# Kernel optimization log

Hardware: AMD Instinct MI355X
Metric: run time of the kernel (lower is better)

The kernel has to match this reference:

```python
import jax, jax.numpy as jnp
import numpy as np
import math

B, N, H, NH, L, NC = 8, 128, 128, 4, 4, 1
DH = H // NH
EPS = 1e-5

def _gelu(x):
    return jax.nn.gelu(x, approximate=False)  # torch nn.GELU default is exact erf

def _ln(x, g, b):
    m = x.mean(-1, keepdims=True)
    v = ((x - m) ** 2).mean(-1, keepdims=True)
    return (x - m) / jnp.sqrt(v + EPS) * g + b

def _bn(x, mask, g, b):
    # BatchNorm1d over valid (unpadded) nodes only, batch statistics (train mode)
    m = mask[..., None].astype(x.dtype)
    cnt = m.sum()
    mu = (x * m).sum((0, 1)) / cnt
    var = (((x - mu) ** 2) * m).sum((0, 1)) / cnt
    return (x - mu) / jnp.sqrt(var + EPS) * g + b

def _forward(e, u, atom_emb, bond_emb, eigw_W, eigw_b, mha_norm_g, mha_norm_b, qkv_W, qkv_b, out_W, out_b, ffn_norm_g, ffn_norm_b, ffn1_W, ffn1_b, ffn2_W, ffn2_b, dec_W, dec_b, fe1_W, fe1_b, fe2_W, fe2_b, pre_W, pre_b, f1_W, f1_b, bn1_g, bn1_b, f2_W, f2_b, bn2_g, bn2_b, lin_W, lin_b, node_feat, edge_feat, length):
    Bx, Nx = e.shape
    node_mask = jnp.arange(Nx)[None, :] < length[:, None]                        # [B,N]
    edge_mask = (node_mask[:, :, None] & node_mask[:, None, :]).astype(e.dtype)  # [B,src,dst]
    # SineEncoding
    div = jnp.exp(jnp.arange(0, H, 2, dtype=e.dtype) * (-math.log(10000.0) / H))
    pe = (e * 100.0)[:, :, None] * div
    eeig = jnp.concatenate([e[..., None], jnp.sin(pe), jnp.cos(pe)], axis=-1)    # [B,N,H+1]
    eig = eeig @ eigw_W.T + eigw_b                                               # [B,N,H]
    # multi-head self-attention over eigenvalue tokens with key padding mask
    xm = _ln(eig, mha_norm_g, mha_norm_b)
    qkv = xm @ qkv_W.T + qkv_b
    q, k, v = jnp.split(qkv, 3, axis=-1)
    q = q.reshape(Bx, Nx, NH, DH).transpose(0, 2, 1, 3)
    k = k.reshape(Bx, Nx, NH, DH).transpose(0, 2, 1, 3)
    v = v.reshape(Bx, Nx, NH, DH).transpose(0, 2, 1, 3)
    scores = jnp.einsum('bhqd,bhkd->bhqk', q, k) / math.sqrt(DH)
    scores = jnp.where(node_mask[:, None, None, :], scores, -jnp.inf)
    attn = jax.nn.softmax(scores, axis=-1)                                       # [B,NH,N,N]
    ctx = jnp.einsum('bhqk,bhkd->bhqd', attn, v).transpose(0, 2, 1, 3).reshape(Bx, Nx, H)
    eig = eig + (ctx @ out_W.T + out_b)
    y = _ln(eig, ffn_norm_g, ffn_norm_b)
    y = _gelu(y @ ffn1_W.T + ffn1_b) @ ffn2_W.T + ffn2_b
    eig = eig + y
    new_e = (eig @ dec_W.T + dec_b).transpose(0, 2, 1)                           # [B,NH,N]
    # spectral bases: identity + u @ diag(new_e_k) @ u^T per head, as fused diagonal scale
    filters = jnp.einsum('bnm,bkm,bpm->bnpk', u, new_e, u)                       # [B,N,N,NH]
    eye = jnp.broadcast_to(jnp.eye(Nx, dtype=e.dtype)[None, :, :, None], (Bx, Nx, Nx, 1))
    bases = jnp.concatenate([eye, filters], axis=-1)                             # [B,N,N,NH+1]
    bases = _gelu(_gelu(bases @ fe1_W.T + fe1_b) @ fe2_W.T + fe2_b)              # [B,N,N,H]
    xf = atom_emb[node_feat]                                                     # [B,N,H]
    ea = bond_emb[edge_feat]                                                     # [B,N,N,H]
    for l in range(L):
        # copy_u gather + per-edge FFN * bases + masked scatter-sum to dst
        msg = _gelu((xf[:, :, None, :] + ea) @ pre_W[l].T + pre_b[l]) * bases
        aggr = jnp.einsum('bijh,bij->bjh', msg, edge_mask)
        xf = xf + aggr
        y = xf @ f1_W[l].T + f1_b[l]
        y = jax.nn.relu(_bn(y, node_mask, bn1_g[l], bn1_b[l]))
        y = y @ f2_W[l].T + f2_b[l]
        y = jax.nn.relu(_bn(y, node_mask, bn2_g[l], bn2_b[l]))
        xf = xf + y
    nm = node_mask[..., None].astype(e.dtype)
    h = (xf * nm).sum(1) / length[:, None].astype(e.dtype)                       # AvgPooling over valid nodes
    h = h @ lin_W.T + lin_b
    return h, new_e, attn

def setup_inputs():
    key = jax.random.key(0)
    ks = iter(jax.random.split(key, 64))
    def w(*shape):
        return jax.random.normal(next(ks), shape, dtype=jnp.float32) * 0.02
    z = lambda *s: jnp.zeros(s, dtype=jnp.float32)
    o = lambda *s: jnp.ones(s, dtype=jnp.float32)
    e = jax.random.uniform(next(ks), (B, N), dtype=jnp.float32) * 2.0
    u = jnp.linalg.qr(jax.random.normal(next(ks), (B, N, N), dtype=jnp.float32))[0]
    inp = {
        'e': e, 'u': u,
        'atom_emb': w(40, H), 'bond_emb': w(10, H).at[0].set(0.0),
        'eigw_W': w(H, H + 1), 'eigw_b': z(H),
        'mha_norm_g': o(H), 'mha_norm_b': z(H),
        'qkv_W': w(3 * H, H), 'qkv_b': z(3 * H),
        'out_W': w(H, H), 'out_b': z(H),
        'ffn_norm_g': o(H), 'ffn_norm_b': z(H),
        'ffn1_W': w(H, H), 'ffn1_b': z(H),
        'ffn2_W': w(H, H), 'ffn2_b': z(H),
        'dec_W': w(NH, H), 'dec_b': z(NH),
        'fe1_W': w(H, NH + 1), 'fe1_b': z(H),
        'fe2_W': w(H, H), 'fe2_b': z(H),
        'pre_W': w(L, H, H), 'pre_b': z(L, H),
        'f1_W': w(L, H, H), 'f1_b': z(L, H),
        'bn1_g': o(L, H), 'bn1_b': z(L, H),
        'f2_W': w(L, H, H), 'f2_b': z(L, H),
        'bn2_g': o(L, H), 'bn2_b': z(L, H),
        'lin_W': w(NC, H), 'lin_b': z(NC),
        'node_feat': jax.random.randint(next(ks), (B, N), 0, 40),
        'edge_feat': jax.random.randint(next(ks), (B, N, N), 0, 10),
        'length': 64 + jax.random.randint(next(ks), (B,), 0, N - 63),
    }
    return inp

def reference(e, u, atom_emb, bond_emb, eigw_W, eigw_b, mha_norm_g, mha_norm_b, qkv_W, qkv_b, out_W, out_b, ffn_norm_g, ffn_norm_b, ffn1_W, ffn1_b, ffn2_W, ffn2_b, dec_W, dec_b, fe1_W, fe1_b, fe2_W, fe2_b, pre_W, pre_b, f1_W, f1_b, bn1_g, bn1_b, f2_W, f2_b, bn2_g, bn2_b, lin_W, lin_b, node_feat, edge_feat, length):
    return _forward(e, u, atom_emb, bond_emb, eigw_W, eigw_b, mha_norm_g, mha_norm_b, qkv_W, qkv_b, out_W, out_b, ffn_norm_g, ffn_norm_b, ffn1_W, ffn1_b, ffn2_W, ffn2_b, dec_W, dec_b, fe1_W, fe1_b, fe2_W, fe2_b, pre_W, pre_b, f1_W, f1_b, bn1_g, bn1_b, f2_W, f2_b, bn2_g, bn2_b, lin_W, lin_b, node_feat, edge_feat, length)
```

## Files before the change

### kernel.cpp

```cpp
#include <hip/hip_runtime.h>
#include <hip/hip_bf16.h>
#include <math.h>

#define BB 8
#define NN 128
#define HH 128
#define NHD 4
#define DHD 32
#define LAY 4
#define EPSV 1e-5f

typedef __hip_bfloat16 bf16;
typedef unsigned short ushortt;
typedef short bf16x8 __attribute__((ext_vector_type(8)));
typedef float f32x4 __attribute__((ext_vector_type(4)));

__device__ __forceinline__ float b2f(bf16 x){ return __bfloat162float(x); }
__device__ __forceinline__ bf16 f2b(float x){ return __float2bfloat16(x); }
__device__ __forceinline__ ushortt f2us(float x){ bf16 b=__float2bfloat16(x); return *(ushortt*)&b; }
__device__ __forceinline__ float gelu_f(float x){ return 0.5f*x*(1.0f+erff(x*0.7071067811865476f)); }
__device__ __forceinline__ float gelu_h(float x){
  float t = 0.7978845608028654f*x*(1.0f + 0.044715f*x*x);
  float e = __expf(2.0f*t);
  float th = 1.0f - 2.0f/(e + 1.0f);
  return 0.5f*x*(1.0f + th);
}
__device__ __forceinline__ float erf_fast(float x){
  float ax = fabsf(x);
  float t = __builtin_amdgcn_rcpf(__builtin_fmaf(0.3275911f, ax, 1.0f));
  float p = __builtin_fmaf(1.061405429f, t, -1.453152027f);
  p = __builtin_fmaf(p, t, 1.421413741f);
  p = __builtin_fmaf(p, t, -0.284496736f);
  p = __builtin_fmaf(p, t, 0.254829592f);
  p = p*t;
  float e = __expf(-ax*ax);
  float y = __builtin_fmaf(-p, e, 1.0f);
  return __builtin_copysignf(y, x);
}
__device__ __forceinline__ float gelu_fe(float x){
  return 0.5f*x*(1.0f + erf_fast(x*0.7071067811865476f));
}


__global__ __launch_bounds__(256) void k_prep(const float* __restrict__ fe2W,
    const float* __restrict__ preW, const float* __restrict__ eigW,
    const float* __restrict__ qkvW, const float* __restrict__ outW,
    const float* __restrict__ ffn1W, const float* __restrict__ ffn2W,
    const float* __restrict__ f1W, const float* __restrict__ f2W,
    const float* __restrict__ aemb, const int* __restrict__ nf,
    const float* __restrict__ bemb, const float* __restrict__ preb,
    ushortt* __restrict__ wbf, float* __restrict__ gs, float* __restrict__ xf0,
    float* __restrict__ eigWT, float* __restrict__ qkvWT, float* __restrict__ outWT,
    float* __restrict__ ffn1WT, float* __restrict__ ffn2WT,
    float* __restrict__ f1WT, float* __restrict__ f2WT,
    float* __restrict__ bondWall){
  int idx = blockIdx.x*256 + threadIdx.x;
  if (idx < 10240) gs[idx] = 0.f;
  if (idx < 81920){
    float v = (idx < 16384) ? fe2W[idx] : preW[idx - 16384];
    wbf[idx] = f2us(v);
  }
  if (idx < 131072){
    int node = idx >> 7, h2 = idx & 127;
    xf0[idx] = aemb[nf[node]*HH + h2];
  }
  if (idx < 16512){ int o = idx/129, kq = idx - o*129; eigWT[kq*128+o] = eigW[idx]; }
  if (idx < 49152){ int o = idx>>7, m = idx&127; qkvWT[m*384+o] = qkvW[idx]; }
  if (idx < 16384){ int o = idx>>7, m = idx&127;
    outWT[m*128+o]  = outW[idx];
    ffn1WT[m*128+o] = ffn1W[idx];
    ffn2WT[m*128+o] = ffn2W[idx];
  }
  if (idx < 65536){ int l = idx>>14, r = idx&16383; int o = r>>7, m = r&127;
    f1WT[l*16384 + m*128+o] = f1W[idx];
    f2WT[l*16384 + m*128+o] = f2W[idx];
  }
  if (idx < 5120){
    int l = idx / 1280; int r = idx - l*1280; int e2 = r >> 7; int hcol = r & 127;
    const float* br = bemb + e2*128;
    const float* wr = preW + l*16384 + hcol*128;
    float acc = preb[l*128 + hcol];
    for (int m=0;m<128;m++) acc += br[m]*wr[m];
    bondWall[idx] = acc;
  }
}


__global__ void k_fe_a(const float* __restrict__ e, const float* __restrict__ eigWT,
                       const float* __restrict__ eigb, const float* __restrict__ g,
                       const float* __restrict__ bt, const float* __restrict__ qkvWT,
                       const float* __restrict__ qkvb,
                       float* __restrict__ eigout, float* __restrict__ q,
                       float* __restrict__ kT, float* __restrict__ v){
  int row = blockIdx.x; int tid = threadIdx.x;
  int b = row >> 7, n = row & 127;
  __shared__ float ee[129]; __shared__ float buf[128]; __shared__ float xm[128];
  float ev = e[row];
  if (tid < 64){
    float dv = expf(-0.1439115683121279f * (float)tid);
    float pe = ev * 100.0f * dv;
    ee[1+tid] = sinf(pe);
    ee[65+tid] = cosf(pe);
  }
  if (tid == 0) ee[0] = ev;
  __syncthreads();
  float x = eigb[tid];
  for (int k2=0;k2<129;k2++) x += ee[k2]*eigWT[k2*128+tid];
  eigout[row*HH+tid] = x;
  buf[tid]=x; __syncthreads();
  for (int s2=64;s2>0;s2>>=1){ if(tid<s2) buf[tid]+=buf[tid+s2]; __syncthreads(); }
  float mean = buf[0]*(1.0f/128.0f); __syncthreads();
  float d = x-mean; buf[tid]=d*d; __syncthreads();
  for (int s2=64;s2>0;s2>>=1){ if(tid<s2) buf[tid]+=buf[tid+s2]; __syncthreads(); }
  float var = buf[0]*(1.0f/128.0f);
  xm[tid] = d*rsqrtf(var+EPSV)*g[tid]+bt[tid];
  __syncthreads();
  #pragma unroll
  for (int s3=0;s3<3;s3++){
    float acc = qkvb[s3*HH+tid];
    const float* wt = qkvWT + s3*HH + tid;
    for (int m=0;m<HH;m++) acc += xm[m]*wt[m*384];
    if (s3==0) q[row*HH+tid]=acc;
    else if (s3==1) kT[b*16384 + tid*128 + n]=acc;
    else v[row*HH+tid]=acc;
  }
}

__global__ __launch_bounds__(512) void k_attc(const float* __restrict__ q,
    const float* __restrict__ kT, const float* __restrict__ v,
    const float* __restrict__ eig, const int* __restrict__ length,
    const float* __restrict__ outWT, const float* __restrict__ outb,
    const float* __restrict__ fng, const float* __restrict__ fnb,
    const float* __restrict__ w1T, const float* __restrict__ b1,
    const float* __restrict__ w2T, const float* __restrict__ b2,
    const float* __restrict__ dW, const float* __restrict__ db,
    float* __restrict__ newe, float* __restrict__ outp){
  int row = blockIdx.x; int b = row>>7, qi = row&127;
  int tid = threadIdx.x;
  int hg = tid>>7, lt = tid&127;
  int len = length[b];
  __shared__ float qv[4][DHD];
  __shared__ float red[4][128];
  __shared__ float satt[4][128];
  __shared__ float sc[128], sbuf[128], sxm[128], stt[128], sx[128];
  if (lt < DHD) qv[hg][lt] = q[(b*NN+qi)*HH + hg*DHD + lt];
  __syncthreads();
  float s = -1e30f;
  if (lt < len){
    const float* kr = kT + b*16384 + hg*DHD*128 + lt;
    float scr=0.f;
    for (int d2=0; d2<DHD; d2++) scr += qv[hg][d2]*kr[d2*128];
    s = scr * 0.17677669529663687f;
  }
  red[hg][lt]=s; __syncthreads();
  for (int st=64;st>0;st>>=1){ if(lt<st) red[hg][lt]=fmaxf(red[hg][lt],red[hg][lt+st]); __syncthreads(); }
  float mx = red[hg][0]; __syncthreads();
  float pp = (lt<len)? expf(s-mx):0.0f;
  red[hg][lt]=pp; __syncthreads();
  for (int st=64;st>0;st>>=1){ if(lt<st) red[hg][lt]+=red[hg][lt+st]; __syncthreads(); }
  float a = pp / red[hg][0];
  satt[hg][lt] = a;
  outp[4104 + ((b*NHD+hg)*NN+qi)*NN + lt] = a;
  __syncthreads();
  if (tid < 128){
    int hd = tid>>5;
    float acc=0.f;
    for (int j=0;j<NN;j++) acc += satt[hd][j]*v[(b*NN+j)*HH+tid];
    sc[tid]=acc;
  }
  __syncthreads();
  if (tid < 128){
    float o = outb[tid];
    for (int m=0;m<HH;m++) o += sc[m]*outWT[m*128+tid];
    float x = eig[row*HH+tid] + o;
    sx[tid] = x; sbuf[tid] = x;
  }
  __syncthreads();
  for (int s2=64;s2>0;s2>>=1){ if(tid<s2) sbuf[tid]+=sbuf[tid+s2]; __syncthreads(); }
  float mean = sbuf[0]*(1.f/128.f); __syncthreads();
  if (tid < 128){ float d = sx[tid]-mean; sbuf[tid]=d*d; }
  __syncthreads();
  for (int s2=64;s2>0;s2>>=1){ if(tid<s2) sbuf[tid]+=sbuf[tid+s2]; __syncthreads(); }
  float var = sbuf[0]*(1.f/128.f);
  if (tid < 128){
    float d = sx[tid]-mean;
    sxm[tid] = d*rsqrtf(var+EPSV)*fng[tid]+fnb[tid];
  }
  __syncthreads();
  if (tid < 128){
    float a1=b1[tid];
    for (int m=0;m<HH;m++) a1+=sxm[m]*w1T[m*128+tid];
    stt[tid]=gelu_f(a1);
  }
  __syncthreads();
  if (tid < 128){
    float a2=b2[tid];
    for (int m=0;m<HH;m++) a2+=stt[m]*w2T[m*128+tid];
    sx[tid] = sx[tid] + a2;
  }
  __syncthreads();
  if (tid < 4){
    float acc = db[tid];
    const float* wr = dW + tid*HH;
    for (int h2=0;h2<HH;h2++) acc += sx[h2]*wr[h2];
    int idx=(b*NHD+tid)*NN+qi;
    newe[idx]=acc; outp[8+idx]=acc;
  }
}

__global__ __launch_bounds__(256) void k_fe2(const float* __restrict__ u,
    const float* __restrict__ newe,
    const float* __restrict__ w1g, const float* __restrict__ b1g,
    const ushortt* __restrict__ w2bf, const float* __restrict__ b2g,
    const int* __restrict__ length,
    bf16* __restrict__ bases){
  int blk = blockIdx.x;
  int bi = blk >> 1;
  int r0 = (blk & 1)*64;
  int b = bi >> 7;
  int nloc = bi & 127;
  int len = length[b];
  if (nloc >= len || r0 >= len) return;
  int tid = threadIdx.x;
  int lane = tid & 63, w = tid >> 6, quad = lane >> 4, l15 = lane & 15;
  int pr = r0 + w*16 + l15;
  __shared__ alignas(16) ushortt sW2[128*128];
  __shared__ float w1a[128*4];
  __shared__ float w1b[128*2];
  __shared__ float b2s[128];
  __shared__ float cn[4][128];
  for (int idx = tid; idx < 2048; idx += 256){
    int r = idx >> 4, cb = idx & 15;
    *(uint4*)&sW2[r*128 + ((cb*8) ^ ((r&15)<<3))] = *(const uint4*)&w2bf[r*128 + cb*8];
  }
  if (tid < 128){
    w1a[tid*4+0] = b1g[tid];
    w1a[tid*4+1] = w1g[tid*5+0];
    w1a[tid*4+2] = w1g[tid*5+1];
    w1a[tid*4+3] = w1g[tid*5+2];
    w1b[tid*2+0] = w1g[tid*5+3];
    w1b[tid*2+1] = w1g[tid*5+4];
    b2s[tid] = b2g[tid];
  }
  for (int idx = tid; idx < 512; idx += 256){
    int k = idx >> 7, m = idx & 127;
    cn[k][m] = u[(b*NN+nloc)*NN + m] * newe[(b*NHD+k)*NN + m];
  }
  __syncthreads();
  bool wact = (r0 + w*16) < len;
  f32x4 acc[8];
  #pragma unroll
  for (int nt=0;nt<8;nt++) acc[nt] = (f32x4){0.f,0.f,0.f,0.f};
  if (wact){
    float f0=0.f, f1=0.f, f2v=0.f, f3=0.f;
    const float4* ur = (const float4*)(u + ((size_t)b*NN + pr)*NN);
    for (int m4 = quad*8; m4 < quad*8+8; m4++){
      float4 uv = ur[m4];
      int m = m4*4;
      f0 += cn[0][m]*uv.x; f0 += cn[0][m+1]*uv.y; f0 += cn[0][m+2]*uv.z; f0 += cn[0][m+3]*uv.w;
      f1 += cn[1][m]*uv.x; f1 += cn[1][m+1]*uv.y; f1 += cn[1][m+2]*uv.z; f1 += cn[1][m+3]*uv.w;
      f2v += cn[2][m]*uv.x; f2v += cn[2][m+1]*uv.y; f2v += cn[2][m+2]*uv.z; f2v += cn[2][m+3]*uv.w;
      f3 += cn[3][m]*uv.x; f3 += cn[3][m+1]*uv.y; f3 += cn[3][m+2]*uv.z; f3 += cn[3][m+3]*uv.w;
    }
    f0 += __shfl_xor(f0, 16, 64);  f0 += __shfl_xor(f0, 32, 64);
    f1 += __shfl_xor(f1, 16, 64);  f1 += __shfl_xor(f1, 32, 64);
    f2v += __shfl_xor(f2v, 16, 64); f2v += __shfl_xor(f2v, 32, 64);
    f3 += __shfl_xor(f3, 16, 64);  f3 += __shfl_xor(f3, 32, 64);
    float dg = (pr == nloc) ? 1.0f : 0.0f;
    for (int kk = 0; kk < 128; kk += 32){
      bf16x8 af;
      #pragma unroll
      for (int j=0;j<8;j++){
        int m = kk + quad*8 + j;
        const float4 wa = *(const float4*)&w1a[m*4];
        const float2 wb = *(const float2*)&w1b[m*2];
        float a = wa.x + wa.y*dg + wa.z*f0 + wa.w*f1 + wb.x*f2v + wb.y*f3;
        af[j] = (short)f2us(gelu_fe(a));
      }
      #pragma unroll
      for (int nt=0;nt<8;nt++){
        int rowb = nt*16 + l15;
        int off = (kk + quad*8) ^ (l15 << 3);
        bf16x8 bfr = *(const bf16x8*)&sW2[rowb*128 + off];
        acc[nt] = __builtin_amdgcn_mfma_f32_16x16x32_bf16(af, bfr, acc[nt], 0, 0, 0);
      }
    }
  }
  __syncthreads();
  ushortt* sT = sW2;
  if (wact){
    #pragma unroll
    for (int nt=0;nt<8;nt++){
      int h = nt*16 + l15;
      float bb = b2s[h];
      #pragma unroll
      for (int reg=0;reg<4;reg++){
        int lr = w*16 + quad*4 + reg;
        sT[lr*132 + h] = f2us(gelu_fe(acc[nt][reg] + bb));
      }
    }
  }
  __syncthreads();
  int rmax = len - r0; if (rmax > 64) rmax = 64;
  ushort4* gout = (ushort4*)(bases + (size_t)bi*16384 + r0*128);
  for (int idx = tid; idx < rmax*32; idx += 256){
    int row = idx >> 5, seg = idx & 31;
    gout[idx] = *(const ushort4*)&sT[row*132 + seg*4];
  }
}


__global__ __launch_bounds__(256) void k_xwl2(const float* __restrict__ xfprev,
    const float* __restrict__ t2, const float* __restrict__ gsum2p,
    const float* __restrict__ gsq2p, const float* __restrict__ g2p,
    const float* __restrict__ bb2p, const int* __restrict__ length, int prevapply,
    const ushortt* __restrict__ wbfl, float* __restrict__ xfB,
    float* __restrict__ xfW){
  int blk = blockIdx.x;
  int b = blk >> 2, rq = blk & 3;
  int tid = threadIdx.x;
  int lane = tid & 63, w = tid >> 6, quad = lane >> 4, l15 = lane & 15;
  __shared__ alignas(16) ushortt sA[32*136];
  __shared__ float smu[128], sistd[128], sg[128], sbb[128];
  if (prevapply && tid < 128){
    float cnt = 0.f;
    for (int q2=0;q2<BB;q2++) cnt += (float)length[q2];
    float mu = gsum2p[tid]/cnt;
    float var = gsq2p[tid]/cnt - mu*mu;
    smu[tid]=mu; sistd[tid]=rsqrtf(fmaxf(var,0.0f)+EPSV);
    sg[tid]=g2p[tid]; sbb[tid]=bb2p[tid];
  }
  __syncthreads();
  for (int idx = tid; idx < 1024; idx += 256){
    int r = idx >> 5, c = idx & 31;
    int gr = b*128 + rq*32 + r;
    float4 xv = ((const float4*)xfprev)[gr*32 + c];
    if (prevapply){
      float4 tv = ((const float4*)t2)[gr*32 + c];
      int f0 = c*4;
      xv.x += fmaxf((tv.x-smu[f0+0])*sistd[f0+0]*sg[f0+0]+sbb[f0+0], 0.f);
      xv.y += fmaxf((tv.y-smu[f0+1])*sistd[f0+1]*sg[f0+1]+sbb[f0+1], 0.f);
      xv.z += fmaxf((tv.z-smu[f0+2])*sistd[f0+2]*sg[f0+2]+sbb[f0+2], 0.f);
      xv.w += fmaxf((tv.w-smu[f0+3])*sistd[f0+3]*sg[f0+3]+sbb[f0+3], 0.f);
      ((float4*)xfB)[gr*32 + c] = xv;
    }
    ushort4 o;
    o.x=f2us(xv.x); o.y=f2us(xv.y); o.z=f2us(xv.z); o.w=f2us(xv.w);
    *(ushort4*)&sA[r*136 + c*4] = o;
  }
  __syncthreads();
  f32x4 acc[2][2];
  #pragma unroll
  for (int mt=0;mt<2;mt++)
    #pragma unroll
    for (int nt=0;nt<2;nt++) acc[mt][nt] = (f32x4){0.f,0.f,0.f,0.f};
  #pragma unroll
  for (int kk = 0; kk < 128; kk += 32){
    bf16x8 af[2], bfr[2];
    #pragma unroll
    for (int mt=0;mt<2;mt++) af[mt] = *(const bf16x8*)&sA[(mt*16+l15)*136 + kk + quad*8];
    #pragma unroll
    for (int nt=0;nt<2;nt++) bfr[nt] = *(const bf16x8*)&wbfl[((w*2+nt)*16+l15)*128 + kk + quad*8];
    #pragma unroll
    for (int mt=0;mt<2;mt++)
      #pragma unroll
      for (int nt=0;nt<2;nt++)
        acc[mt][nt] = __builtin_amdgcn_mfma_f32_16x16x32_bf16(af[mt], bfr[nt], acc[mt][nt], 0, 0, 0);
  }
  #pragma unroll
  for (int mt=0;mt<2;mt++)
    #pragma unroll
    for (int nt=0;nt<2;nt++){
      int h = (w*2+nt)*16 + l15;
      #pragma unroll
      for (int reg=0;reg<4;reg++){
        int prr = rq*32 + mt*16 + quad*4 + reg;
        xfW[(b*128 + prr)*128 + h] = acc[mt][nt][reg];
      }
    }
}

__global__ __launch_bounds__(512) void k_edge(const float* __restrict__ xfin, float* __restrict__ xfout,
    const bf16* __restrict__ bases, const float* __restrict__ xfW,
    const float* __restrict__ bondWl, const int* __restrict__ ef,
    const int* __restrict__ length,
    const float* __restrict__ w1t, const float* __restrict__ bias1,
    float* __restrict__ t1, float* __restrict__ gst){
  int bj = blockIdx.x; int b = bj >> 7, j = bj & 127;
  int len = length[b];
  int tid = threadIdx.x; int h = tid & 127, ih = tid >> 7;
  __shared__ float sBW[10][128];
  __shared__ int sEf[128];
  __shared__ float part[4][128];
  for (int idx = tid; idx < 1280; idx += 512) sBW[idx>>7][idx&127] = bondWl[idx];
  if (tid < 128) sEf[tid] = ef[(b*NN + tid)*NN + j];
  __syncthreads();
  float agg = 0.f;
  if (j < len){
    const float* xwb = xfW + b*NN*HH + h;
    const bf16* bb = bases + ((size_t)b*NN + j)*NN*HH + h;
    for (int i = ih; i < len; i += 4){
      float vv = gelu_h(xwb[i*128] + sBW[sEf[i]][h]);
      agg += vv * b2f(bb[i*128]);
    }
  }
  part[ih][h] = agg; __syncthreads();
  if (tid < 128){
    int o = (b*NN + j)*HH + tid;
    float xrow = xfin[o] + part[0][tid] + part[1][tid] + part[2][tid] + part[3][tid];
    xfout[o] = xrow;
    part[0][tid] = xrow;
  }
  __syncthreads();
  float acc = (ih==0) ? bias1[h] : 0.f;
  {
    const float* wcol = w1t + h;
    int m0 = ih*32;
    for (int m = m0; m < m0+32; m++) acc += part[0][m]*wcol[m*128];
  }
  float* red = &sBW[0][0];
  __syncthreads();
  red[ih*128 + h] = acc; __syncthreads();
  if (tid < 128){
    float t1v = red[tid] + red[128+tid] + red[256+tid] + red[384+tid];
    t1[(b*NN + j)*HH + tid] = t1v;
    if (j < len){
      int bank = bj & 7;
      atomicAdd(&gst[bank*256 + tid], t1v);
      atomicAdd(&gst[bank*256 + 128 + tid], t1v*t1v);
    }
  }
}

__global__ __launch_bounds__(256) void k_g2s(const float* __restrict__ t1,
    const float* __restrict__ gstL,
    const float* __restrict__ g1, const float* __restrict__ bb1,
    const float* __restrict__ w2t, const float* __restrict__ bias2,
    const int* __restrict__ length, float* __restrict__ t2){
  int blk = blockIdx.x; int tid = threadIdx.x;
  int f = tid & 127, rh = tid >> 7;
  __shared__ float sy[4][128];
  __shared__ float red1[2][128], red2[2][128];
  int r0 = blk*4;
  float cnt = 0.f;
  for (int b=0;b<BB;b++) cnt += (float)length[b];
  float su = 0.f, sq = 0.f;
  #pragma unroll
  for (int k=0;k<8;k++){ su += gstL[k*256 + f]; sq += gstL[k*256 + 128 + f]; }
  float mu = su/cnt;
  float var = sq/cnt - mu*mu;
  float istd = rsqrtf(fmaxf(var,0.0f)+EPSV);
  float gg = g1[f], bbv = bb1[f];
  for (int idx = tid; idx < 512; idx += 256){
    int r = idx >> 7;
    float x = t1[(r0+r)*128 + f];
    float y = (x-mu)*istd*gg + bbv;
    sy[r][f] = fmaxf(y, 0.0f);
  }
  __syncthreads();
  float bsv = bias2[f];
  float s=0.f, s2=0.f;
  for (int rr = rh*2; rr < rh*2+2; rr++){
    int rg = r0 + rr; int b = rg >> 7, n = rg & 127;
    float acc = bsv;
    for (int m=0;m<128;m++) acc += sy[rr][m]*w2t[m*128+f];
    t2[rg*128+f] = acc;
    if (n < length[b]){ s += acc; s2 += acc*acc; }
  }
  red1[rh][f]=s; red2[rh][f]=s2; __syncthreads();
  if (tid < 128){
    atomicAdd((float*)&gstL[2048 + tid], red1[0][tid]+red1[1][tid]);
    atomicAdd((float*)&gstL[2048 + 128 + tid], red2[0][tid]+red2[1][tid]);
  }
}

__global__ void k_pool2(const float* __restrict__ xf, const float* __restrict__ t2,
                        const float* __restrict__ gsum2, const float* __restrict__ gsq2,
                        const float* __restrict__ g2, const float* __restrict__ bb2,
                        const int* __restrict__ length,
                        const float* lw, const float* lb, float* __restrict__ outp){
  int b = blockIdx.x, tid=threadIdx.x;
  int len = length[b];
  float cnt = 0.f;
  for (int q2=0;q2<BB;q2++) cnt += (float)length[q2];
  float mu = gsum2[tid]/cnt;
  float var = gsq2[tid]/cnt - mu*mu;
  float istd = rsqrtf(fmaxf(var,0.0f)+EPSV);
  float gg = g2[tid], bbv = bb2[tid];
  float s=0.f;
  for (int n2=0;n2<len;n2++){
    int o = (b*NN+n2)*HH+tid;
    float x = xf[o] + fmaxf((t2[o]-mu)*istd*gg+bbv, 0.0f);
    s += x;
  }
  s /= (float)len;
  __shared__ float red[128];
  red[tid]=s*lw[tid]; __syncthreads();
  for (int st=64;st>0;st>>=1){ if(tid<st) red[tid]+=red[tid+st]; __syncthreads(); }
  if (tid==0) outp[b]=red[0]+lb[0];
}


extern "C" void kernel_launch(void* const* d_in, const int* in_sizes, int n_in,
                              void* d_out, int out_size, void* d_ws, size_t ws_size,
                              hipStream_t stream) {
  (void)in_sizes; (void)n_in; (void)out_size; (void)ws_size;
  const float* e        = (const float*)d_in[0];
  const float* u        = (const float*)d_in[1];
  const float* atom_emb = (const float*)d_in[2];
  const float* bond_emb = (const float*)d_in[3];
  const float* eigw_W   = (const float*)d_in[4];
  const float* eigw_b   = (const float*)d_in[5];
  const float* mng      = (const float*)d_in[6];
  const float* mnb      = (const float*)d_in[7];
  const float* qkvW     = (const float*)d_in[8];
  const float* qkvb     = (const float*)d_in[9];
  const float* outW     = (const float*)d_in[10];
  const float* outb     = (const float*)d_in[11];
  const float* fng      = (const float*)d_in[12];
  const float* fnb      = (const float*)d_in[13];
  const float* ffn1W    = (const float*)d_in[14];
  const float* ffn1b    = (const float*)d_in[15];
  const float* ffn2W    = (const float*)d_in[16];
  const float* ffn2b    = (const float*)d_in[17];
  const float* decW     = (const float*)d_in[18];
  const float* decb     = (const float*)d_in[19];
  const float* fe1W     = (const float*)d_in[20];
  const float* fe1b     = (const float*)d_in[21];
  const float* fe2W     = (const float*)d_in[22];
  const float* fe2b     = (const float*)d_in[23];
  const float* preW     = (const float*)d_in[24];
  const float* preb     = (const float*)d_in[25];
  const float* f1W      = (const float*)d_in[26];
  const float* f1b      = (const float*)d_in[27];
  const float* bn1g     = (const float*)d_in[28];
  const float* bn1b     = (const float*)d_in[29];
  const float* f2W      = (const float*)d_in[30];
  const float* f2b      = (const float*)d_in[31];
  const float* bn2g     = (const float*)d_in[32];
  const float* bn2b     = (const float*)d_in[33];
  const float* linW     = (const float*)d_in[34];
  const float* linb     = (const float*)d_in[35];
  const int* nodef      = (const int*)d_in[36];
  const int* edgef      = (const int*)d_in[37];
  const int* length     = (const int*)d_in[38];

  float* outp = (float*)d_out;

  char* p = (char*)d_ws;
  auto alloc = [&](size_t bytes)->void*{ void* r=(void*)p; p += (bytes+255)&~(size_t)255; return r; };
  const int TOK = BB*NN*HH;
  float* eig   = (float*)alloc(TOK*4);
  float* q     = (float*)alloc(TOK*4);
  float* kT    = (float*)alloc(TOK*4);
  float* v     = (float*)alloc(TOK*4);
  float* newe  = (float*)alloc(BB*NHD*NN*4);
  bf16*  bases = (bf16*) alloc((size_t)BB*NN*NN*HH*2);
  float* xf0   = (float*)alloc(TOK*4);
  float* xfB   = (float*)alloc(TOK*4);
  float* xfC   = (float*)alloc(TOK*4);
  float* xfD   = (float*)alloc(TOK*4);
  float* t1    = (float*)alloc(TOK*4);
  float* t2    = (float*)alloc(TOK*4);
  float* xfW   = (float*)alloc(TOK*4);
  float* gs    = (float*)alloc(10240*4);
  ushortt* wbf = (ushortt*)alloc(81920*2);
  float* eigWT = (float*)alloc(16512*4);
  float* qkvWT = (float*)alloc(49152*4);
  float* outWT = (float*)alloc(16384*4);
  float* ffn1WT= (float*)alloc(16384*4);
  float* ffn2WT= (float*)alloc(16384*4);
  float* f1WT  = (float*)alloc(65536*4);
  float* f2WT  = (float*)alloc(65536*4);
  float* bondWall = (float*)alloc(5120*4);

  k_prep<<<512, 256, 0, stream>>>(fe2W, preW, eigw_W, qkvW, outW, ffn1W, ffn2W,
                                  f1W, f2W, atom_emb, nodef, bond_emb, preb,
                                  wbf, gs, xf0, eigWT, qkvWT, outWT, ffn1WT,
                                  ffn2WT, f1WT, f2WT, bondWall);

  k_fe_a<<<BB*NN, 128, 0, stream>>>(e, eigWT, eigw_b, mng, mnb, qkvWT, qkvb, eig, q, kT, v);
  k_attc<<<BB*NN, 512, 0, stream>>>(q, kT, v, eig, length,
                                    outWT, outb, fng, fnb,
                                    ffn1WT, ffn1b, ffn2WT, ffn2b,
                                    decW, decb, newe, outp);

  k_fe2<<<2*BB*NN, 256, 0, stream>>>(u, newe, fe1W, fe1b, wbf, fe2b, length, bases);

  const float* xfprev = xf0;
  float* xfcur = xfC;
  for (int l=0;l<LAY;l++){
    const ushortt* wbfl = wbf + 16384 + l*16384;
    float* gsl = gs + l*2560;
    float* gsp = gs + (l-1)*2560;
    k_xwl2<<<BB*4, 256, 0, stream>>>(xfprev, t2,
                                   (l>0)? gsp+2048 : gs, (l>0)? gsp+2048+128 : gs,
                                   bn2g + (l>0? (l-1)*HH:0), bn2b + (l>0? (l-1)*HH:0),
                                   length, (l>0)?1:0,
                                   wbfl, xfB, xfW);
    const float* xin = (l==0)? xf0 : xfB;
    k_edge<<<BB*NN, 512, 0, stream>>>(xin, xfcur, bases, xfW, bondWall + l*1280,
                                      edgef, length,
                                      f1WT + l*16384, f1b + l*HH, t1, gsl);
    k_g2s<<<256, 256, 0, stream>>>(t1, gsl, bn1g + l*HH, bn1b + l*HH,
                                   f2WT + l*16384, f2b + l*HH, length, t2);
    xfprev = xfcur;
    xfcur = (xfcur == xfC) ? xfD : xfC;
  }
  k_pool2<<<BB, 128, 0, stream>>>(xfprev, t2, gs+3*2560+2048, gs+3*2560+2048+128,
                                  bn2g + 3*HH, bn2b + 3*HH, length, linW, linb, outp);
}
```

Before: 399.4 us.

## Fuse per-layer node transform GEMM into edge aggregation kernel with recomputation

Merges k_xwl2 into k_edge, so each of the 1024 edge blocks recomputes the full 128x128 X·W GEMM for its graph in shared memory, together with the previous layer's BN-ReLU residual. This removes one launch per layer and the global round trips through xfB and xfW. In exchange, the GEMM work is redundantly repeated 128 times per graph and each block uses about 64KB of shared memory, which limits occupancy.

After: 532.3 us. 33.3% more time.

```diff
diff --git a/kernel.cpp b/kernel.cpp
--- a/kernel.cpp
+++ b/kernel.cpp
@@ -310,18 +310,31 @@
 }
 
 
-__global__ __launch_bounds__(256) void k_xwl2(const float* __restrict__ xfprev,
+__global__ __launch_bounds__(512) void k_edgeX(const float* __restrict__ xfprev,
     const float* __restrict__ t2, const float* __restrict__ gsum2p,
     const float* __restrict__ gsq2p, const float* __restrict__ g2p,
-    const float* __restrict__ bb2p, const int* __restrict__ length, int prevapply,
-    const ushortt* __restrict__ wbfl, float* __restrict__ xfB,
-    float* __restrict__ xfW){
-  int blk = blockIdx.x;
-  int b = blk >> 2, rq = blk & 3;
+    const float* __restrict__ bb2p, int prevapply,
+    const ushortt* __restrict__ wbfl, const float* __restrict__ bondWl,
+    const bf16* __restrict__ bases, const int* __restrict__ ef,
+    const int* __restrict__ length,
+    const float* __restrict__ w1t, const float* __restrict__ bias1,
+    float* __restrict__ xfout, float* __restrict__ t1, float* __restrict__ gst){
+  int bj = blockIdx.x; int b = bj >> 7, j = bj & 127;
+  int len = length[b];
   int tid = threadIdx.x;
   int lane = tid & 63, w = tid >> 6, quad = lane >> 4, l15 = lane & 15;
-  __shared__ alignas(16) ushortt sA[32*136];
+  int h = tid & 127, ih = tid >> 7;
+
+  __shared__ alignas(16) char uSpace[65536];
+  ushortt* sA = (ushortt*)uSpace;
+  float* sXW = (float*)uSpace;
+  __shared__ float sBW[1280];
+  __shared__ int sEf[128];
+  __shared__ float part[4][128];
+  __shared__ float red[4][128];
+  __shared__ float sXin[128];
   __shared__ float smu[128], sistd[128], sg[128], sbb[128];
+
   if (prevapply && tid < 128){
     float cnt = 0.f;
     for (int q2=0;q2<BB;q2++) cnt += (float)length[q2];
@@ -330,99 +343,72 @@
     smu[tid]=mu; sistd[tid]=rsqrtf(fmaxf(var,0.0f)+EPSV);
     sg[tid]=g2p[tid]; sbb[tid]=bb2p[tid];
   }
-  __syncthreads();
-  for (int idx = tid; idx < 1024; idx += 256){
+  for (int idx = tid; idx < 1280; idx += 512) sBW[idx] = bondWl[idx];
+  if (tid < 128) sEf[tid] = ef[(b*NN + tid)*NN + j];
+  __syncthreads();
+  for (int idx = tid; idx < 4096; idx += 512){
     int r = idx >> 5, c = idx & 31;
-    int gr = b*128 + rq*32 + r;
-    float4 xv = ((const float4*)xfprev)[gr*32 + c];
+    float4 xv = ((const float4*)xfprev)[(b*128 + r)*32 + c];
     if (prevapply){
-      float4 tv = ((const float4*)t2)[gr*32 + c];
+      float4 tv = ((const float4*)t2)[(b*128 + r)*32 + c];
       int f0 = c*4;
       xv.x += fmaxf((tv.x-smu[f0+0])*sistd[f0+0]*sg[f0+0]+sbb[f0+0], 0.f);
       xv.y += fmaxf((tv.y-smu[f0+1])*sistd[f0+1]*sg[f0+1]+sbb[f0+1], 0.f);
       xv.z += fmaxf((tv.z-smu[f0+2])*sistd[f0+2]*sg[f0+2]+sbb[f0+2], 0.f);
       xv.w += fmaxf((tv.w-smu[f0+3])*sistd[f0+3]*sg[f0+3]+sbb[f0+3], 0.f);
-      ((float4*)xfB)[gr*32 + c] = xv;
-    }
+    }
+    if (r == j) ((float4*)sXin)[c] = xv;
     ushort4 o;
     o.x=f2us(xv.x); o.y=f2us(xv.y); o.z=f2us(xv.z); o.w=f2us(xv.w);
     *(ushort4*)&sA[r*136 + c*4] = o;
   }
   __syncthreads();
-  f32x4 acc[2][2];
+  f32x4 acc[8];
   #pragma unroll
-  for (int mt=0;mt<2;mt++)
-    #pragma unroll
-    for (int nt=0;nt<2;nt++) acc[mt][nt] = (f32x4){0.f,0.f,0.f,0.f};
+  for (int nt=0;nt<8;nt++) acc[nt] = (f32x4){0.f,0.f,0.f,0.f};
   #pragma unroll
   for (int kk = 0; kk < 128; kk += 32){
-    bf16x8 af[2], bfr[2];
+    bf16x8 af = *(const bf16x8*)&sA[(w*16+l15)*136 + kk + quad*8];
     #pragma unroll
-    for (int mt=0;mt<2;mt++) af[mt] = *(const bf16x8*)&sA[(mt*16+l15)*136 + kk + quad*8];
+    for (int nt=0;nt<8;nt++){
+      bf16x8 bfr = *(const bf16x8*)&wbfl[(nt*16+l15)*128 + kk + quad*8];
+      acc[nt] = __builtin_amdgcn_mfma_f32_16x16x32_bf16(af, bfr, acc[nt], 0, 0, 0);
+    }
+  }
+  __syncthreads();
+  #pragma unroll
+  for (int nt=0;nt<8;nt++){
     #pragma unroll
-    for (int nt=0;nt<2;nt++) bfr[nt] = *(const bf16x8*)&wbfl[((w*2+nt)*16+l15)*128 + kk + quad*8];
-    #pragma unroll
-    for (int mt=0;mt<2;mt++)
-      #pragma unroll
-      for (int nt=0;nt<2;nt++)
-        acc[mt][nt] = __builtin_amdgcn_mfma_f32_16x16x32_bf16(af[mt], bfr[nt], acc[mt][nt], 0, 0, 0);
-  }
-  #pragma unroll
-  for (int mt=0;mt<2;mt++)
-    #pragma unroll
-    for (int nt=0;nt<2;nt++){
-      int h = (w*2+nt)*16 + l15;
-      #pragma unroll
-      for (int reg=0;reg<4;reg++){
-        int prr = rq*32 + mt*16 + quad*4 + reg;
-        xfW[(b*128 + prr)*128 + h] = acc[mt][nt][reg];
-      }
-    }
-}
-
-__global__ __launch_bounds__(512) void k_edge(const float* __restrict__ xfin, float* __restrict__ xfout,
-    const bf16* __restrict__ bases, const float* __restrict__ xfW,
-    const float* __restrict__ bondWl, const int* __restrict__ ef,
-    const int* __restrict__ length,
-    const float* __restrict__ w1t, const float* __restrict__ bias1,
-    float* __restrict__ t1, float* __restrict__ gst){
-  int bj = blockIdx.x; int b = bj >> 7, j = bj & 127;
-  int len = length[b];
-  int tid = threadIdx.x; int h = tid & 127, ih = tid >> 7;
-  __shared__ float sBW[10][128];
-  __shared__ int sEf[128];
-  __shared__ float part[4][128];
-  for (int idx = tid; idx < 1280; idx += 512) sBW[idx>>7][idx&127] = bondWl[idx];
-  if (tid < 128) sEf[tid] = ef[(b*NN + tid)*NN + j];
+    for (int reg=0;reg<4;reg++){
+      sXW[(w*16 + quad*4 + reg)*128 + nt*16 + l15] = acc[nt][reg];
+    }
+  }
   __syncthreads();
   float agg = 0.f;
   if (j < len){
-    const float* xwb = xfW + b*NN*HH + h;
     const bf16* bb = bases + ((size_t)b*NN + j)*NN*HH + h;
     for (int i = ih; i < len; i += 4){
-      float vv = gelu_h(xwb[i*128] + sBW[sEf[i]][h]);
+      float vv = gelu_h(sXW[i*128 + h] + sBW[sEf[i]*128 + h]);
       agg += vv * b2f(bb[i*128]);
     }
   }
   part[ih][h] = agg; __syncthreads();
   if (tid < 128){
     int o = (b*NN + j)*HH + tid;
-    float xrow = xfin[o] + part[0][tid] + part[1][tid] + part[2][tid] + part[3][tid];
+    float xrow = sXin[tid] + part[0][tid] + part[1][tid] + part[2][tid] + part[3][tid];
     xfout[o] = xrow;
     part[0][tid] = xrow;
   }
   __syncthreads();
-  float acc = (ih==0) ? bias1[h] : 0.f;
+  float acc1 = (ih==0) ? bias1[h] : 0.f;
   {
     const float* wcol = w1t + h;
     int m0 = ih*32;
-    for (int m = m0; m < m0+32; m++) acc += part[0][m]*wcol[m*128];
-  }
-  float* red = &sBW[0][0];
-  __syncthreads();
-  red[ih*128 + h] = acc; __syncthreads();
-  if (tid < 128){
-    float t1v = red[tid] + red[128+tid] + red[256+tid] + red[384+tid];
+    for (int m = m0; m < m0+32; m++) acc1 += part[0][m]*wcol[m*128];
+  }
+  red[ih][h] = acc1; __syncthreads();
+  if (tid < 128){
+    float t1v = red[0][tid] + red[1][tid] + red[2][tid] + red[3][tid];
     t1[(b*NN + j)*HH + tid] = t1v;
     if (j < len){
       int bank = bj & 7;
@@ -557,12 +543,10 @@
   float* newe  = (float*)alloc(BB*NHD*NN*4);
   bf16*  bases = (bf16*) alloc((size_t)BB*NN*NN*HH*2);
   float* xf0   = (float*)alloc(TOK*4);
-  float* xfB   = (float*)alloc(TOK*4);
   float* xfC   = (float*)alloc(TOK*4);
   float* xfD   = (float*)alloc(TOK*4);
   float* t1    = (float*)alloc(TOK*4);
   float* t2    = (float*)alloc(TOK*4);
-  float* xfW   = (float*)alloc(TOK*4);
   float* gs    = (float*)alloc(10240*4);
   ushortt* wbf = (ushortt*)alloc(81920*2);
   float* eigWT = (float*)alloc(16512*4);
@@ -593,15 +577,13 @@
     const ushortt* wbfl = wbf + 16384 + l*16384;
     float* gsl = gs + l*2560;
     float* gsp = gs + (l-1)*2560;
-    k_xwl2<<<BB*4, 256, 0, stream>>>(xfprev, t2,
-                                   (l>0)? gsp+2048 : gs, (l>0)? gsp+2048+128 : gs,
-                                   bn2g + (l>0? (l-1)*HH:0), bn2b + (l>0? (l-1)*HH:0),
-                                   length, (l>0)?1:0,
-                                   wbfl, xfB, xfW);
-    const float* xin = (l==0)? xf0 : xfB;
-    k_edge<<<BB*NN, 512, 0, stream>>>(xin, xfcur, bases, xfW, bondWall + l*1280,
-                                      edgef, length,
-                                      f1WT + l*16384, f1b + l*HH, t1, gsl);
+    k_edgeX<<<BB*NN, 512, 0, stream>>>(xfprev, t2,
+                                       (l>0)? gsp+2048 : gs, (l>0)? gsp+2048+128 : gs,
+                                       bn2g + (l>0? (l-1)*HH:0), bn2b + (l>0? (l-1)*HH:0),
+                                       (l>0)?1:0,
+                                       wbfl, bondWall + l*1280, bases, edgef, length,
+                                       f1WT + l*16384, f1b + l*HH,
+                                       xfcur, t1, gsl);
     k_g2s<<<256, 256, 0, stream>>>(t1, gsl, bn1g + l*HH, bn1b + l*HH,
                                    f2WT + l*16384, f2b + l*HH, length, t2);
     xfprev = xfcur;
```
